# Optimization experiments

Hardware: AMD Instinct MI355X
Metric: run time of the kernel (lower is better)

## Reference

```python
import jax, jax.numpy as jnp
import numpy as np

B, P = 4, 65536
TD, HID, OUT = 32, 128, 4
RES = 256
NFREQ = 6
CD = 3 * 2 * NFREQ  # frequency encoding out dim


def setup_inputs() -> dict:
    key = jax.random.key(0)
    ks = jax.random.split(key, 12)

    def w(k, shape):
        fan_in = shape[-1]
        return jax.random.normal(k, shape, jnp.float32) / np.sqrt(fan_in)

    return {
        "triplane": jax.random.normal(ks[0], (3 * B, TD, RES, RES), jnp.float32),
        "coords": jax.random.uniform(ks[1], (B, P, 3), jnp.float32),  # inside aabb [-1,1]^3
        "w_in": w(ks[2], (HID, TD + CD)),
        "b_in": jnp.zeros((HID,), jnp.float32),
        "w_skip": w(ks[3], (HID, TD + CD)),
        "b_skip": jnp.zeros((HID,), jnp.float32),
        "w_before": w(ks[4], (2, HID, HID)),
        "b_before": jnp.zeros((2, HID), jnp.float32),
        "w_after": w(ks[5], (2, HID, HID)),
        "b_after": jnp.zeros((2, HID), jnp.float32),
        "w_out": w(ks[6], (OUT, HID)),
        "b_out": jnp.zeros((OUT,), jnp.float32),
    }


@jax.custom_vjp
def trunc_exp(x):
    return jnp.exp(x)


def _trunc_exp_fwd(x):
    return jnp.exp(x), x


def _trunc_exp_bwd(x, g):
    return (g * jnp.exp(jnp.clip(x, -15.0, 15.0)),)


trunc_exp.defvjp(_trunc_exp_fwd, _trunc_exp_bwd)


def grid_sample_bilinear(feat, gx, gy):
    # feat: [N, C, H, W]; gx, gy: [N, Q] in [-1, 1]; align_corners=True, zero padding.
    N, C, H, W = feat.shape
    ix = (gx + 1.0) * 0.5 * (W - 1)
    iy = (gy + 1.0) * 0.5 * (H - 1)
    x0 = jnp.floor(ix)
    y0 = jnp.floor(iy)
    wx1 = ix - x0
    wy1 = iy - y0
    feat_flat = feat.reshape(N, C, H * W)

    def gather(xf, yf):
        xi = xf.astype(jnp.int32)
        yi = yf.astype(jnp.int32)
        valid = ((xi >= 0) & (xi < W) & (yi >= 0) & (yi < H)).astype(feat.dtype)
        xi = jnp.clip(xi, 0, W - 1)
        yi = jnp.clip(yi, 0, H - 1)
        idx = yi * W + xi  # [N, Q]
        g = jnp.take_along_axis(feat_flat, idx[:, None, :], axis=2)  # [N, C, Q]
        return g * valid[:, None, :]

    out = (
        gather(x0, y0) * ((1 - wx1) * (1 - wy1))[:, None, :]
        + gather(x0 + 1, y0) * (wx1 * (1 - wy1))[:, None, :]
        + gather(x0, y0 + 1) * ((1 - wx1) * wy1)[:, None, :]
        + gather(x0 + 1, y0 + 1) * (wx1 * wy1)[:, None, :]
    )
    return out  # [N, C, Q]


def freq_encode(x):
    # x: [B, P, 3] in [0, 1]; NeRF-style frequency encoding (tcnn 'Frequency').
    freqs = (2.0 ** jnp.arange(NFREQ, dtype=x.dtype)) * jnp.pi  # [NFREQ]
    ang = x[..., :, None] * freqs  # [B, P, 3, NFREQ]
    enc = jnp.concatenate([jnp.sin(ang), jnp.cos(ang)], axis=-1)  # [B, P, 3, 2*NFREQ]
    return enc.reshape(x.shape[0], x.shape[1], CD)


def reference(triplane, coords, w_in, b_in, w_skip, b_skip, w_before, b_before,
              w_after, b_after, w_out, b_out):
    aabb_min = jnp.full((3,), -1.0, jnp.float32)
    aabb_max = jnp.full((3,), 1.0, jnp.float32)

    scaled = 2.0 * (coords - aabb_min) / (aabb_max - aabb_min) - 1.0  # [-1,1]
    norm = (coords - aabb_min) / (aabb_max - aabb_min)  # [0,1]
    selector = jnp.all((norm > 0.0) & (norm < 1.0), axis=-1)  # [B, P]

    # planes: xy=(x,y), xz=(x,z), zy=(y,z); stacked per batch -> [3B, P, 2]
    coords_xy = scaled[:, :, (0, 1)]
    coords_xz = scaled[:, :, (0, 2)]
    coords_zy = scaled[:, :, (1, 2)]
    grid = jnp.stack([coords_xy, coords_xz, coords_zy], axis=1).reshape(3 * B, P, 2)

    feats = grid_sample_bilinear(triplane, grid[..., 0], grid[..., 1])  # [3B, TD, P]
    feats = feats.transpose(0, 2, 1).reshape(B, 3, P, TD).sum(axis=1)  # [B, P, TD]

    h = jnp.concatenate([freq_encode(norm), feats], axis=-1)  # [B, P, CD+TD]

    lin = lambda x, w, b: jnp.einsum("bpf,hf->bph", x, w) + b
    x = jax.nn.relu(lin(h, w_in, b_in))
    for i in range(w_before.shape[0]):
        x = jax.nn.relu(lin(x, w_before[i], b_before[i]))
    x = x + jax.nn.relu(lin(h, w_skip, b_skip))
    for i in range(w_after.shape[0]):
        x = jax.nn.relu(lin(x, w_after[i], b_after[i]))
    x = lin(x, w_out, b_out)  # [B, P, 4]

    rgb = jax.nn.sigmoid(x[..., :3])
    density = trunc_exp(x[..., 3:4] - 1.0) * selector[..., None].astype(x.dtype)
    return rgb, density
```

## Files before the change

kernel.cpp:

```cpp
#include <hip/hip_runtime.h>
#include <stdint.h>

typedef short short8 __attribute__((ext_vector_type(8)));
typedef float floatx16 __attribute__((ext_vector_type(16)));
typedef unsigned int uint32;

#define NPTS (4 * 65536)
#define RGB_OFF (NPTS * 3)

__device__ __forceinline__ uint16_t bf_rne(float f) {
  uint32 u = __float_as_uint(f);
  u += 0x7FFFu + ((u >> 16) & 1u);
  return (uint16_t)(u >> 16);
}
__device__ __forceinline__ uint32 pack2(float a, float b) {
  return __builtin_amdgcn_perm(__float_as_uint(b) + 0x8000u,
                               __float_as_uint(a) + 0x8000u, 0x07060302u);
}
__device__ __forceinline__ float bf_lo(uint32 u) { return __uint_as_float(u << 16); }
__device__ __forceinline__ float bf_hi(uint32 u) { return __uint_as_float(u & 0xFFFF0000u); }
__device__ __forceinline__ void swap32(uint32& a, uint32& b) {
  asm("v_permlane32_swap_b32 %0, %1" : "+v"(a), "+v"(b));
}
__device__ __forceinline__ void gacc(const uint16_t* p, float w, float* acc) {
  uint4 q = *(const uint4*)p;
  acc[0] += w * bf_lo(q.x);
  acc[1] += w * bf_hi(q.x);
  acc[2] += w * bf_lo(q.y);
  acc[3] += w * bf_hi(q.y);
  acc[4] += w * bf_lo(q.z);
  acc[5] += w * bf_hi(q.z);
  acc[6] += w * bf_lo(q.w);
  acc[7] += w * bf_hi(q.w);
}

__global__ __launch_bounds__(256) void k_prep(
    const float* __restrict__ tri, uint16_t* __restrict__ out, int ntr,
    const float* __restrict__ w_in, const float* __restrict__ w_skip,
    const float* __restrict__ w_before, const float* __restrict__ w_after,
    const float* __restrict__ w_out, const float* __restrict__ b_in,
    const float* __restrict__ b_skip, const float* __restrict__ b_before,
    const float* __restrict__ b_after, const float* __restrict__ b_out,
    uint16_t* __restrict__ wpack, float* __restrict__ bpack) {
  const int bx = blockIdx.x;
  if (bx < ntr) {
    const size_t P = (size_t)bx * 256 + threadIdx.x;
    const int n = (int)(P >> 16);
    const int rem = (int)(P & 65535);
    const float* src = tri + ((size_t)n << 21) + rem;
    uint32 q[16];
#pragma unroll
    for (int c = 0; c < 16; ++c) {
      float a = src[(size_t)(2 * c) << 16];
      float b = src[(size_t)(2 * c + 1) << 16];
      q[c] = pack2(a, b);
    }
    uint4* dst = (uint4*)(out + P * 32);
    dst[0] = make_uint4(q[0], q[1], q[2], q[3]);
    dst[1] = make_uint4(q[4], q[5], q[6], q[7]);
    dst[2] = make_uint4(q[8], q[9], q[10], q[11]);
    dst[3] = make_uint4(q[12], q[13], q[14], q[15]);
    return;
  }
  const int blk = bx - ntr;
  if (blk >= 44) {
    for (int t = threadIdx.x; t < 800; t += 256) {
      int l, idx;
      if (t < 768) { l = t >> 7; idx = t & 127; }
      else { l = 6; idx = t - 768; }
      int mt = idx >> 5, rem = idx & 31;
      int half = rem >> 4, r = rem & 15;
      int f = mt * 32 + (r & 3) + 8 * (r >> 2) + 4 * half;
      float v;
      switch (l) {
        case 0: v = b_in[f]; break;
        case 1: v = b_before[f]; break;
        case 2: v = b_before[128 + f]; break;
        case 3: v = b_skip[f]; break;
        case 4: v = b_after[f]; break;
        case 5: v = b_after[128 + f]; break;
        default: v = (f < 4) ? b_out[f] : 0.0f; break;
      }
      bpack[l * 128 + idx] = v;
    }
    return;
  }
  const int w = blk * 4 + (threadIdx.x >> 6);
  const int L = threadIdx.x & 63;
  int lay, mt, k;
  if (w < 20)      { lay = 0; mt = w / 5;        k = w - mt * 5; }
  else if (w < 52) { int u = w - 20;  lay = 1; mt = u >> 3; k = u & 7; }
  else if (w < 84) { int u = w - 52;  lay = 2; mt = u >> 3; k = u & 7; }
  else if (w < 104){ int u = w - 84;  lay = 3; mt = u / 5;  k = u - mt * 5; }
  else if (w < 136){ int u = w - 104; lay = 4; mt = u >> 3; k = u & 7; }
  else if (w < 168){ int u = w - 136; lay = 5; mt = u >> 3; k = u & 7; }
  else             { lay = 6; mt = 0; k = w - 168; }
  const float* W;
  int insk = 0;
  switch (lay) {
    case 0: W = w_in; insk = 1; break;
    case 1: W = w_before; break;
    case 2: W = w_before + 16384; break;
    case 3: W = w_skip; insk = 1; break;
    case 4: W = w_after; break;
    case 5: W = w_after + 16384; break;
    default: W = w_out; break;
  }
  const int frow = mt * 32 + (L & 31);
  const int kbase = k * 16 + (L >> 5) * 8;
  uint16_t h[8];
#pragma unroll
  for (int j = 0; j < 8; ++j) {
    int kl = kbase + j;
    float v;
    if (insk) {
      int col = (kl < 32) ? (36 + kl) : ((kl < 68) ? (kl - 32) : -1);
      v = (col < 0) ? 0.0f : W[frow * 68 + col];
    } else if (lay == 6) {
      v = (frow < 4) ? W[frow * 128 + kl] : 0.0f;
    } else {
      v = W[frow * 128 + kl];
    }
    h[j] = bf_rne(v);
  }
  uint4 q;
  q.x = (uint32)h[0] | ((uint32)h[1] << 16);
  q.y = (uint32)h[2] | ((uint32)h[3] << 16);
  q.z = (uint32)h[4] | ((uint32)h[5] << 16);
  q.w = (uint32)h[6] | ((uint32)h[7] << 16);
  *(uint4*)(wpack + (size_t)w * 512 + L * 8) = q;
}

__device__ __forceinline__ void gather_encode(const uint16_t* __restrict__ trit,
                                              const float* __restrict__ coords,
                                              int pg, int kh, uint4* hq,
                                              bool* selp) {
  float cx = coords[pg * 3 + 0], cy = coords[pg * 3 + 1], cz = coords[pg * 3 + 2];
  float f1x = cx + 1.0f, f1y = cy + 1.0f, f1z = cz + 1.0f;
  float nx = f1x * 0.5f, ny = f1y * 0.5f, nz = f1z * 0.5f;
  float sx = f1x - 1.0f, sy = f1y - 1.0f, sz = f1z - 1.0f;
  *selp = (nx > 0.f) & (nx < 1.f) & (ny > 0.f) & (ny < 1.f) & (nz > 0.f) & (nz < 1.f);
  const int b = pg >> 16;
  float acc[16];
#pragma unroll
  for (int j = 0; j < 16; ++j) acc[j] = 0.f;
#pragma unroll
  for (int pl = 0; pl < 3; ++pl) {
    float gx = (pl == 2) ? sy : sx;
    float gy = (pl == 0) ? sy : sz;
    float ix = ((gx + 1.0f) * 0.5f) * 255.0f;
    float iy = ((gy + 1.0f) * 0.5f) * 255.0f;
    float x0f = floorf(ix), y0f = floorf(iy);
    float wx = ix - x0f, wy = iy - y0f;
    float vx0 = (x0f >= 0.0f && x0f < 256.0f) ? 1.f : 0.f;
    float vx1 = (x0f >= -1.0f && x0f < 255.0f) ? 1.f : 0.f;
    float vy0 = (y0f >= 0.0f && y0f < 256.0f) ? 1.f : 0.f;
    float vy1 = (y0f >= -1.0f && y0f < 255.0f) ? 1.f : 0.f;
    int x0 = min(max((int)x0f, 0), 255), x1 = min(max((int)x0f + 1, 0), 255);
    int y0 = min(max((int)y0f, 0), 255), y1 = min(max((int)y0f + 1, 0), 255);
    float w00 = (1.f - wx) * (1.f - wy) * vx0 * vy0;
    float w10 = wx * (1.f - wy) * vx1 * vy0;
    float w01 = (1.f - wx) * wy * vx0 * vy1;
    float w11 = wx * wy * vx1 * vy1;
    const int n = 3 * b + pl;
    const uint16_t* cb = trit + ((size_t)n << 21) + kh * 8;
    size_t o00 = (size_t)(y0 * 256 + x0) << 5, o10 = (size_t)(y0 * 256 + x1) << 5;
    size_t o01 = (size_t)(y1 * 256 + x0) << 5, o11 = (size_t)(y1 * 256 + x1) << 5;
    gacc(cb + o00, w00, acc); gacc(cb + 16 + o00, w00, acc + 8);
    gacc(cb + o10, w10, acc); gacc(cb + 16 + o10, w10, acc + 8);
    gacc(cb + o01, w01, acc); gacc(cb + 16 + o01, w01, acc + 8);
    gacc(cb + o11, w11, acc); gacc(cb + 16 + o11, w11, acc + 8);
  }
  hq[0] = make_uint4(pack2(acc[0], acc[1]), pack2(acc[2], acc[3]),
                     pack2(acc[4], acc[5]), pack2(acc[6], acc[7]));
  hq[1] = make_uint4(pack2(acc[8], acc[9]), pack2(acc[10], acc[11]),
                     pack2(acc[12], acc[13]), pack2(acc[14], acc[15]));
  float sv[3][6], cv[3][6];
#pragma unroll
  for (int d = 0; d < 3; ++d) {
    float nd = (d == 0) ? nx : (d == 1) ? ny : nz;
#pragma unroll
    for (int k = 0; k < 6; ++k) {
      float rev = nd * (0.5f * (float)(1 << k));
      float r = rev - rintf(rev);
      sv[d][k] = __builtin_amdgcn_sinf(r);
      cv[d][k] = __builtin_amdgcn_cosf(r);
    }
  }
  if (kh == 0) {
    hq[2] = make_uint4(pack2(sv[0][0], sv[0][1]), pack2(sv[0][2], sv[0][3]),
                       pack2(sv[0][4], sv[0][5]), pack2(cv[0][0], cv[0][1]));
    hq[3] = make_uint4(pack2(sv[1][4], sv[1][5]), pack2(cv[1][0], cv[1][1]),
                       pack2(cv[1][2], cv[1][3]), pack2(cv[1][4], cv[1][5]));
    hq[4] = make_uint4(pack2(cv[2][2], cv[2][3]), pack2(cv[2][4], cv[2][5]), 0u, 0u);
  } else {
    hq[2] = make_uint4(pack2(cv[0][2], cv[0][3]), pack2(cv[0][4], cv[0][5]),
                       pack2(sv[1][0], sv[1][1]), pack2(sv[1][2], sv[1][3]));
    hq[3] = make_uint4(pack2(sv[2][0], sv[2][1]), pack2(sv[2][2], sv[2][3]),
                       pack2(sv[2][4], sv[2][5]), pack2(cv[2][0], cv[2][1]));
    hq[4] = make_uint4(0u, 0u, 0u, 0u);
  }
}

template <int BASE, int LAY, int Ks>
__device__ __forceinline__ void mfma_block(floatx16* a, const short8* bin,
                                           const uint16_t* __restrict__ wpack,
                                           const float* __restrict__ bpack, int L,
                                           int kh) {
#pragma unroll
  for (int mt = 0; mt < 4; ++mt) {
    const float4* bp = (const float4*)(bpack + LAY * 128 + mt * 32 + kh * 16);
#pragma unroll
    for (int g = 0; g < 4; ++g) {
      float4 v = bp[g];
      a[mt][4 * g + 0] = v.x; a[mt][4 * g + 1] = v.y;
      a[mt][4 * g + 2] = v.z; a[mt][4 * g + 3] = v.w;
    }
  }
  const uint16_t* wp = wpack + (size_t)BASE * 512 + L * 8;
#pragma unroll
  for (int k = 0; k < Ks; ++k) {
    short8 w0 = *(const short8*)(wp + (size_t)(0 * Ks + k) * 512);
    short8 w1 = *(const short8*)(wp + (size_t)(1 * Ks + k) * 512);
    short8 w2 = *(const short8*)(wp + (size_t)(2 * Ks + k) * 512);
    short8 w3 = *(const short8*)(wp + (size_t)(3 * Ks + k) * 512);
    a[0] = __builtin_amdgcn_mfma_f32_32x32x16_bf16(w0, bin[k], a[0], 0, 0, 0);
    a[1] = __builtin_amdgcn_mfma_f32_32x32x16_bf16(w1, bin[k], a[1], 0, 0, 0);
    a[2] = __builtin_amdgcn_mfma_f32_32x32x16_bf16(w2, bin[k], a[2], 0, 0, 0);
    a[3] = __builtin_amdgcn_mfma_f32_32x32x16_bf16(w3, bin[k], a[3], 0, 0, 0);
  }
}

template <int BASE, int LAY, int Ks>
__device__ __forceinline__ void layer_dense(const short8* bin, short8* bout,
                                            const uint16_t* __restrict__ wpack,
                                            const float* __restrict__ bpack, int L,
                                            int kh) {
  floatx16 a[4];
  mfma_block<BASE, LAY, Ks>(a, bin, wpack, bpack, L, kh);
#pragma unroll
  for (int f = 0; f < 8; ++f) {
    const int mt = f >> 1, s = f & 1;
    uint32 q0a = pack2(fmaxf(a[mt][8 * s + 0], 0.f), fmaxf(a[mt][8 * s + 1], 0.f));
    uint32 q0b = pack2(fmaxf(a[mt][8 * s + 2], 0.f), fmaxf(a[mt][8 * s + 3], 0.f));
    uint32 q1a = pack2(fmaxf(a[mt][8 * s + 4], 0.f), fmaxf(a[mt][8 * s + 5], 0.f));
    uint32 q1b = pack2(fmaxf(a[mt][8 * s + 6], 0.f), fmaxf(a[mt][8 * s + 7], 0.f));
    swap32(q0a, q1a);
    swap32(q0b, q1b);
    bout[f] = __builtin_bit_cast(short8, make_uint4(q0a, q0b, q1a, q1b));
  }
}

template <int BASE, int LAY, int Ks>
__device__ __forceinline__ void layer_skip(const short8* hin, short8* bio,
                                           const uint16_t* __restrict__ wpack,
                                           const float* __restrict__ bpack, int L,
                                           int kh) {
  floatx16 a[4];
  mfma_block<BASE, LAY, Ks>(a, hin, wpack, bpack, L, kh);
#pragma unroll
  for (int f = 0; f < 8; ++f) {
    const int mt = f >> 1, s = f & 1;
    uint4 old = __builtin_bit_cast(uint4, bio[f]);
    uint32 uA = old.x, uB = old.y, uC = old.z, uD = old.w;
    swap32(uA, uC);
    swap32(uB, uD);
    float r0 = fmaxf(a[mt][8 * s + 0], 0.f) + bf_lo(uA);
    float r1 = fmaxf(a[mt][8 * s + 1], 0.f) + bf_hi(uA);
    float r2 = fmaxf(a[mt][8 * s + 2], 0.f) + bf_lo(uB);
    float r3 = fmaxf(a[mt][8 * s + 3], 0.f) + bf_hi(uB);
    float r4 = fmaxf(a[mt][8 * s + 4], 0.f) + bf_lo(uC);
    float r5 = fmaxf(a[mt][8 * s + 5], 0.f) + bf_hi(uC);
    float r6 = fmaxf(a[mt][8 * s + 6], 0.f) + bf_lo(uD);
    float r7 = fmaxf(a[mt][8 * s + 7], 0.f) + bf_hi(uD);
    uint32 q0a = pack2(r0, r1), q0b = pack2(r2, r3);
    uint32 q1a = pack2(r4, r5), q1b = pack2(r6, r7);
    swap32(q0a, q1a);
    swap32(q0b, q1b);
    bio[f] = __builtin_bit_cast(short8, make_uint4(q0a, q0b, q1a, q1b));
  }
}

__device__ __forceinline__ void mlp_body(const short8* hf, bool sel,
                                         const uint16_t* __restrict__ wpack,
                                         const float* __restrict__ bpack,
                                         float* __restrict__ dout, int L, int kh,
                                         int pg) {
  short8 bf[8];
  layer_dense<0, 0, 5>(hf, bf, wpack, bpack, L, kh);
  layer_dense<20, 1, 8>(bf, bf, wpack, bpack, L, kh);
  layer_dense<52, 2, 8>(bf, bf, wpack, bpack, L, kh);
  layer_skip<84, 3, 5>(hf, bf, wpack, bpack, L, kh);
  layer_dense<104, 4, 8>(bf, bf, wpack, bpack, L, kh);
  layer_dense<136, 5, 8>(bf, bf, wpack, bpack, L, kh);

  floatx16 a;
  const float4* bp = (const float4*)(bpack + 768 + kh * 16);
#pragma unroll
  for (int g = 0; g < 4; ++g) {
    float4 v = bp[g];
    a[4 * g + 0] = v.x; a[4 * g + 1] = v.y; a[4 * g + 2] = v.z; a[4 * g + 3] = v.w;
  }
  const uint16_t* wp = wpack + (size_t)168 * 512 + L * 8;
#pragma unroll
  for (int k = 0; k < 8; ++k) {
    short8 af = *(const short8*)(wp + (size_t)k * 512);
    a = __builtin_amdgcn_mfma_f32_32x32x16_bf16(af, bf[k], a, 0, 0, 0);
  }
  if (kh == 0) {
    const float l2e = 1.44269504f;
    float r0 = 1.0f / (1.0f + exp2f(-l2e * a[0]));
    float r1 = 1.0f / (1.0f + exp2f(-l2e * a[1]));
    float r2 = 1.0f / (1.0f + exp2f(-l2e * a[2]));
    float dens = exp2f((a[3] - 1.0f) * l2e) * (sel ? 1.0f : 0.0f);
    dout[pg * 3 + 0] = r0;
    dout[pg * 3 + 1] = r1;
    dout[pg * 3 + 2] = r2;
    dout[RGB_OFF + pg] = dens;
  }
}

__global__ __launch_bounds__(256, 3) void k_main(
    const uint16_t* __restrict__ trit, const float* __restrict__ trif,
    const float* __restrict__ coords, const uint16_t* __restrict__ wpack,
    const float* __restrict__ bpack, float* __restrict__ dout, int fast) {
  const int t = threadIdx.x;
  const int L = t & 63;
  const int kh = L >> 5;
  const int p = (t >> 6) * 32 + (L & 31);
  const int pg = blockIdx.x * 128 + p;

  short8 hf[5];
  bool sel;
  if (fast) {
    uint4 hq[5];
    gather_encode(trit, coords, pg, kh, hq, &sel);
#pragma unroll
    for (int f = 0; f < 5; ++f) hf[f] = __builtin_bit_cast(short8, hq[f]);
  } else {
    float cx = coords[pg * 3 + 0], cy = coords[pg * 3 + 1], cz = coords[pg * 3 + 2];
    float f1x = cx + 1.0f, f1y = cy + 1.0f, f1z = cz + 1.0f;
    float nx = f1x * 0.5f, ny = f1y * 0.5f, nz = f1z * 0.5f;
    float sx = f1x - 1.0f, sy = f1y - 1.0f, sz = f1z - 1.0f;
    sel = (nx > 0.f) & (nx < 1.f) & (ny > 0.f) & (ny < 1.f) & (nz > 0.f) & (nz < 1.f);
    const int b = pg >> 16;
    float acc[16];
#pragma unroll
    for (int j = 0; j < 16; ++j) acc[j] = 0.f;
#pragma unroll
    for (int pl = 0; pl < 3; ++pl) {
      float gx = (pl == 2) ? sy : sx;
      float gy = (pl == 0) ? sy : sz;
      float ix = ((gx + 1.0f) * 0.5f) * 255.0f;
      float iy = ((gy + 1.0f) * 0.5f) * 255.0f;
      float x0f = floorf(ix), y0f = floorf(iy);
      float wx = ix - x0f, wy = iy - y0f;
      float vx0 = (x0f >= 0.0f && x0f < 256.0f) ? 1.f : 0.f;
      float vx1 = (x0f >= -1.0f && x0f < 255.0f) ? 1.f : 0.f;
      float vy0 = (y0f >= 0.0f && y0f < 256.0f) ? 1.f : 0.f;
      float vy1 = (y0f >= -1.0f && y0f < 255.0f) ? 1.f : 0.f;
      int x0 = min(max((int)x0f, 0), 255), x1 = min(max((int)x0f + 1, 0), 255);
      int y0 = min(max((int)y0f, 0), 255), y1 = min(max((int)y0f + 1, 0), 255);
      float w00 = (1.f - wx) * (1.f - wy) * vx0 * vy0;
      float w10 = wx * (1.f - wy) * vx1 * vy0;
      float w01 = (1.f - wx) * wy * vx0 * vy1;
      float w11 = wx * wy * vx1 * vy1;
      const int n = 3 * b + pl;
      const float* basef = trif + (((size_t)n * 32) << 16);
#pragma unroll
      for (int j = 0; j < 8; ++j) {
        const float* c0p = basef + (((size_t)(kh * 8 + j)) << 16);
        const float* c1p = basef + (((size_t)(16 + kh * 8 + j)) << 16);
        acc[j] += w00 * c0p[y0 * 256 + x0] + w10 * c0p[y0 * 256 + x1] +
                  w01 * c0p[y1 * 256 + x0] + w11 * c0p[y1 * 256 + x1];
        acc[8 + j] += w00 * c1p[y0 * 256 + x0] + w10 * c1p[y0 * 256 + x1] +
                      w01 * c1p[y1 * 256 + x0] + w11 * c1p[y1 * 256 + x1];
      }
    }
    hf[0] = __builtin_bit_cast(
        short8, make_uint4(pack2(acc[0], acc[1]), pack2(acc[2], acc[3]),
                           pack2(acc[4], acc[5]), pack2(acc[6], acc[7])));
    hf[1] = __builtin_bit_cast(
        short8, make_uint4(pack2(acc[8], acc[9]), pack2(acc[10], acc[11]),
                           pack2(acc[12], acc[13]), pack2(acc[14], acc[15])));
    float sv[3][6], cv[3][6];
#pragma unroll
    for (int d = 0; d < 3; ++d) {
      float nd = (d == 0) ? nx : (d == 1) ? ny : nz;
#pragma unroll
      for (int k = 0; k < 6; ++k) {
        float rev = nd * (0.5f * (float)(1 << k));
        float r = rev - rintf(rev);
        sv[d][k] = __builtin_amdgcn_sinf(r);
        cv[d][k] = __builtin_amdgcn_cosf(r);
      }
    }
    if (kh == 0) {
      hf[2] = __builtin_bit_cast(
          short8, make_uint4(pack2(sv[0][0], sv[0][1]), pack2(sv[0][2], sv[0][3]),
                             pack2(sv[0][4], sv[0][5]), pack2(cv[0][0], cv[0][1])));
      hf[3] = __builtin_bit_cast(
          short8, make_uint4(pack2(sv[1][4], sv[1][5]), pack2(cv[1][0], cv[1][1]),
                             pack2(cv[1][2], cv[1][3]), pack2(cv[1][4], cv[1][5])));
      hf[4] = __builtin_bit_cast(
          short8, make_uint4(pack2(cv[2][2], cv[2][3]), pack2(cv[2][4], cv[2][5]), 0u, 0u));
    } else {
      hf[2] = __builtin_bit_cast(
          short8, make_uint4(pack2(cv[0][2], cv[0][3]), pack2(cv[0][4], cv[0][5]),
                             pack2(sv[1][0], sv[1][1]), pack2(sv[1][2], sv[1][3])));
      hf[3] = __builtin_bit_cast(
          short8, make_uint4(pack2(sv[2][0], sv[2][1]), pack2(sv[2][2], sv[2][3]),
                             pack2(sv[2][4], sv[2][5]), pack2(cv[2][0], cv[2][1])));
      hf[4] = __builtin_bit_cast(short8, make_uint4(0u, 0u, 0u, 0u));
    }
  }
  mlp_body(hf, sel, wpack, bpack, dout, L, kh, pg);
}

extern "C" void kernel_launch(void* const* d_in, const int* in_sizes, int n_in,
                              void* d_out, int out_size, void* d_ws, size_t ws_size,
                              hipStream_t stream) {
  const float* tri = (const float*)d_in[0];
  const float* coords = (const float*)d_in[1];
  const float* w_in = (const float*)d_in[2];
  const float* b_in = (const float*)d_in[3];
  const float* w_skip = (const float*)d_in[4];
  const float* b_skip = (const float*)d_in[5];
  const float* w_bef = (const float*)d_in[6];
  const float* b_bef = (const float*)d_in[7];
  const float* w_aft = (const float*)d_in[8];
  const float* b_aft = (const float*)d_in[9];
  const float* w_out = (const float*)d_in[10];
  const float* b_out = (const float*)d_in[11];
  const size_t TRI_B = (size_t)12 * 256 * 256 * 32 * 2;
  const size_t WP_B = (size_t)176 * 1024;
  const size_t BP_B = 3200;
  char* ws = (char*)d_ws;
  const int fast = (ws_size >= TRI_B + WP_B + BP_B) ? 1 : 0;
  uint16_t* trit;
  uint16_t* wpk;
  float* bpk;
  if (fast) {
    trit = (uint16_t*)ws;
    wpk = (uint16_t*)(ws + TRI_B);
    bpk = (float*)(ws + TRI_B + WP_B);
  } else {
    trit = (uint16_t*)ws;
    wpk = (uint16_t*)ws;
    bpk = (float*)(ws + WP_B);
  }
  const int ntr = fast ? 3072 : 0;
  k_prep<<<dim3(ntr + 45), dim3(256), 0, stream>>>(
      tri, trit, ntr, w_in, w_skip, w_bef, w_aft, w_out, b_in, b_skip, b_bef,
      b_aft, b_out, wpk, bpk);
  k_main<<<dim3(2048), dim3(256), 0, stream>>>(trit, tri, coords, wpk, bpk,
                                               (float*)d_out, fast);
}
```

Measured before the change: 274.4 us.

## Stage MLP weight fragments through shared memory in phases per block

Packed bf16 MLP weights are copied cooperatively into a 52 KB LDS buffer in several phases, and MFMA operand fragments are read from LDS instead of from global memory. Each of the 4 waves previously fetched the same weight fragments from global/L2 separately. The change adds several __syncthreads barriers and about 52 KB of LDS per block, which may limit occupancy below the 3 blocks per CU requested by the launch bounds. The first stage is issued before the gather so that the copy can overlap with it.

```diff
diff --git a/kernel.cpp b/kernel.cpp
--- a/kernel.cpp
+++ b/kernel.cpp
@@ -129,6 +129,147 @@
   q.z = (uint32)h[4] | ((uint32)h[5] << 16);
   q.w = (uint32)h[6] | ((uint32)h[7] << 16);
   *(uint4*)(wpack + (size_t)w * 512 + L * 8) = q;
+}
+
+template <int NFRAG>
+__device__ __forceinline__ void stage(const uint16_t* __restrict__ wp_base,
+                                      uint16_t* __restrict__ wbuf, int t) {
+#pragma unroll
+  for (int i = 0; i < NFRAG * 64 / 256; ++i) {
+    const int g = t + i * 256;
+    uint4 v = *(const uint4*)(wp_base + g * 8);
+    *(uint4*)(wbuf + g * 8) = v;
+  }
+}
+
+template <int LAY, int Ks>
+__device__ __forceinline__ void mfma_block(floatx16* a, const short8* bin,
+                                           const uint16_t* __restrict__ wbuf,
+                                           const float* __restrict__ bpack, int L,
+                                           int kh) {
+#pragma unroll
+  for (int mt = 0; mt < 4; ++mt) {
+    const float4* bp = (const float4*)(bpack + LAY * 128 + mt * 32 + kh * 16);
+#pragma unroll
+    for (int g = 0; g < 4; ++g) {
+      float4 v = bp[g];
+      a[mt][4 * g + 0] = v.x; a[mt][4 * g + 1] = v.y;
+      a[mt][4 * g + 2] = v.z; a[mt][4 * g + 3] = v.w;
+    }
+  }
+  const uint16_t* wp = wbuf + L * 8;
+#pragma unroll
+  for (int k = 0; k < Ks; ++k) {
+    short8 w0 = *(const short8*)(wp + (size_t)(0 * Ks + k) * 512);
+    short8 w1 = *(const short8*)(wp + (size_t)(1 * Ks + k) * 512);
+    short8 w2 = *(const short8*)(wp + (size_t)(2 * Ks + k) * 512);
+    short8 w3 = *(const short8*)(wp + (size_t)(3 * Ks + k) * 512);
+    a[0] = __builtin_amdgcn_mfma_f32_32x32x16_bf16(w0, bin[k], a[0], 0, 0, 0);
+    a[1] = __builtin_amdgcn_mfma_f32_32x32x16_bf16(w1, bin[k], a[1], 0, 0, 0);
+    a[2] = __builtin_amdgcn_mfma_f32_32x32x16_bf16(w2, bin[k], a[2], 0, 0, 0);
+    a[3] = __builtin_amdgcn_mfma_f32_32x32x16_bf16(w3, bin[k], a[3], 0, 0, 0);
+  }
+}
+
+template <int LAY, int Ks>
+__device__ __forceinline__ void layer_dense(const short8* bin, short8* bout,
+                                            const uint16_t* __restrict__ wbuf,
+                                            const float* __restrict__ bpack, int L,
+                                            int kh) {
+  floatx16 a[4];
+  mfma_block<LAY, Ks>(a, bin, wbuf, bpack, L, kh);
+#pragma unroll
+  for (int f = 0; f < 8; ++f) {
+    const int mt = f >> 1, s = f & 1;
+    uint32 q0a = pack2(fmaxf(a[mt][8 * s + 0], 0.f), fmaxf(a[mt][8 * s + 1], 0.f));
+    uint32 q0b = pack2(fmaxf(a[mt][8 * s + 2], 0.f), fmaxf(a[mt][8 * s + 3], 0.f));
+    uint32 q1a = pack2(fmaxf(a[mt][8 * s + 4], 0.f), fmaxf(a[mt][8 * s + 5], 0.f));
+    uint32 q1b = pack2(fmaxf(a[mt][8 * s + 6], 0.f), fmaxf(a[mt][8 * s + 7], 0.f));
+    swap32(q0a, q1a);
+    swap32(q0b, q1b);
+    bout[f] = __builtin_bit_cast(short8, make_uint4(q0a, q0b, q1a, q1b));
+  }
+}
+
+template <int LAY, int Ks>
+__device__ __forceinline__ void layer_skip(const short8* hin, short8* bio,
+                                           const uint16_t* __restrict__ wbuf,
+                                           const float* __restrict__ bpack, int L,
+                                           int kh) {
+  floatx16 a[4];
+  mfma_block<LAY, Ks>(a, hin, wbuf, bpack, L, kh);
+#pragma unroll
+  for (int f = 0; f < 8; ++f) {
+    const int mt = f >> 1, s = f & 1;
+    uint4 old = __builtin_bit_cast(uint4, bio[f]);
+    uint32 uA = old.x, uB = old.y, uC = old.z, uD = old.w;
+    swap32(uA, uC);
+    swap32(uB, uD);
+    float r0 = fmaxf(a[mt][8 * s + 0], 0.f) + bf_lo(uA);
+    float r1 = fmaxf(a[mt][8 * s + 1], 0.f) + bf_hi(uA);
+    float r2 = fmaxf(a[mt][8 * s + 2], 0.f) + bf_lo(uB);
+    float r3 = fmaxf(a[mt][8 * s + 3], 0.f) + bf_hi(uB);
+    float r4 = fmaxf(a[mt][8 * s + 4], 0.f) + bf_lo(uC);
+    float r5 = fmaxf(a[mt][8 * s + 5], 0.f) + bf_hi(uC);
+    float r6 = fmaxf(a[mt][8 * s + 6], 0.f) + bf_lo(uD);
+    float r7 = fmaxf(a[mt][8 * s + 7], 0.f) + bf_hi(uD);
+    uint32 q0a = pack2(r0, r1), q0b = pack2(r2, r3);
+    uint32 q1a = pack2(r4, r5), q1b = pack2(r6, r7);
+    swap32(q0a, q1a);
+    swap32(q0b, q1b);
+    bio[f] = __builtin_bit_cast(short8, make_uint4(q0a, q0b, q1a, q1b));
+  }
+}
+
+__device__ __forceinline__ void mlp_body(const short8* hf, bool sel,
+                                         const uint16_t* __restrict__ wpack,
+                                         const float* __restrict__ bpack,
+                                         uint16_t* __restrict__ wbuf,
+                                         float* __restrict__ dout, int t, int L,
+                                         int kh, int pg) {
+  short8 bf[8];
+  __syncthreads();
+  layer_dense<0, 5>(hf, bf, wbuf, bpack, L, kh);
+  layer_dense<1, 8>(bf, bf, wbuf + (size_t)20 * 512, bpack, L, kh);
+  __syncthreads();
+  stage<52>(wpack + (size_t)52 * 512, wbuf, t);
+  __syncthreads();
+  layer_dense<2, 8>(bf, bf, wbuf, bpack, L, kh);
+  layer_skip<3, 5>(hf, bf, wbuf + (size_t)32 * 512, bpack, L, kh);
+  __syncthreads();
+  stage<32>(wpack + (size_t)104 * 512, wbuf, t);
+  stage<8>(wpack + (size_t)168 * 512, wbuf + (size_t)32 * 512, t);
+  __syncthreads();
+  layer_dense<4, 8>(bf, bf, wbuf, bpack, L, kh);
+  __syncthreads();
+  stage<32>(wpack + (size_t)136 * 512, wbuf, t);
+  __syncthreads();
+  layer_dense<5, 8>(bf, bf, wbuf, bpack, L, kh);
+
+  floatx16 a;
+  const float4* bp = (const float4*)(bpack + 768 + kh * 16);
+#pragma unroll
+  for (int g = 0; g < 4; ++g) {
+    float4 v = bp[g];
+    a[4 * g + 0] = v.x; a[4 * g + 1] = v.y; a[4 * g + 2] = v.z; a[4 * g + 3] = v.w;
+  }
+  const uint16_t* wp = wbuf + (size_t)32 * 512 + L * 8;
+#pragma unroll
+  for (int k = 0; k < 8; ++k) {
+    short8 af = *(const short8*)(wp + (size_t)k * 512);
+    a = __builtin_amdgcn_mfma_f32_32x32x16_bf16(af, bf[k], a, 0, 0, 0);
+  }
+  if (kh == 0) {
+    const float l2e = 1.44269504f;
+    float r0 = 1.0f / (1.0f + exp2f(-l2e * a[0]));
+    float r1 = 1.0f / (1.0f + exp2f(-l2e * a[1]));
+    float r2 = 1.0f / (1.0f + exp2f(-l2e * a[2]));
+    float dens = exp2f((a[3] - 1.0f) * l2e) * (sel ? 1.0f : 0.0f);
+    dout[pg * 3 + 0] = r0;
+    dout[pg * 3 + 1] = r1;
+    dout[pg * 3 + 2] = r2;
+    dout[RGB_OFF + pg] = dens;
+  }
 }
 
 __device__ __forceinline__ void gather_encode(const uint16_t* __restrict__ trit,
@@ -202,133 +343,18 @@
   }
 }
 
-template <int BASE, int LAY, int Ks>
-__device__ __forceinline__ void mfma_block(floatx16* a, const short8* bin,
-                                           const uint16_t* __restrict__ wpack,
-                                           const float* __restrict__ bpack, int L,
-                                           int kh) {
-#pragma unroll
-  for (int mt = 0; mt < 4; ++mt) {
-    const float4* bp = (const float4*)(bpack + LAY * 128 + mt * 32 + kh * 16);
-#pragma unroll
-    for (int g = 0; g < 4; ++g) {
-      float4 v = bp[g];
-      a[mt][4 * g + 0] = v.x; a[mt][4 * g + 1] = v.y;
-      a[mt][4 * g + 2] = v.z; a[mt][4 * g + 3] = v.w;
-    }
-  }
-  const uint16_t* wp = wpack + (size_t)BASE * 512 + L * 8;
-#pragma unroll
-  for (int k = 0; k < Ks; ++k) {
-    short8 w0 = *(const short8*)(wp + (size_t)(0 * Ks + k) * 512);
-    short8 w1 = *(const short8*)(wp + (size_t)(1 * Ks + k) * 512);
-    short8 w2 = *(const short8*)(wp + (size_t)(2 * Ks + k) * 512);
-    short8 w3 = *(const short8*)(wp + (size_t)(3 * Ks + k) * 512);
-    a[0] = __builtin_amdgcn_mfma_f32_32x32x16_bf16(w0, bin[k], a[0], 0, 0, 0);
-    a[1] = __builtin_amdgcn_mfma_f32_32x32x16_bf16(w1, bin[k], a[1], 0, 0, 0);
-    a[2] = __builtin_amdgcn_mfma_f32_32x32x16_bf16(w2, bin[k], a[2], 0, 0, 0);
-    a[3] = __builtin_amdgcn_mfma_f32_32x32x16_bf16(w3, bin[k], a[3], 0, 0, 0);
-  }
-}
-
-template <int BASE, int LAY, int Ks>
-__device__ __forceinline__ void layer_dense(const short8* bin, short8* bout,
-                                            const uint16_t* __restrict__ wpack,
-                                            const float* __restrict__ bpack, int L,
-                                            int kh) {
-  floatx16 a[4];
-  mfma_block<BASE, LAY, Ks>(a, bin, wpack, bpack, L, kh);
-#pragma unroll
-  for (int f = 0; f < 8; ++f) {
-    const int mt = f >> 1, s = f & 1;
-    uint32 q0a = pack2(fmaxf(a[mt][8 * s + 0], 0.f), fmaxf(a[mt][8 * s + 1], 0.f));
-    uint32 q0b = pack2(fmaxf(a[mt][8 * s + 2], 0.f), fmaxf(a[mt][8 * s + 3], 0.f));
-    uint32 q1a = pack2(fmaxf(a[mt][8 * s + 4], 0.f), fmaxf(a[mt][8 * s + 5], 0.f));
-    uint32 q1b = pack2(fmaxf(a[mt][8 * s + 6], 0.f), fmaxf(a[mt][8 * s + 7], 0.f));
-    swap32(q0a, q1a);
-    swap32(q0b, q1b);
-    bout[f] = __builtin_bit_cast(short8, make_uint4(q0a, q0b, q1a, q1b));
-  }
-}
-
-template <int BASE, int LAY, int Ks>
-__device__ __forceinline__ void layer_skip(const short8* hin, short8* bio,
-                                           const uint16_t* __restrict__ wpack,
-                                           const float* __restrict__ bpack, int L,
-                                           int kh) {
-  floatx16 a[4];
-  mfma_block<BASE, LAY, Ks>(a, hin, wpack, bpack, L, kh);
-#pragma unroll
-  for (int f = 0; f < 8; ++f) {
-    const int mt = f >> 1, s = f & 1;
-    uint4 old = __builtin_bit_cast(uint4, bio[f]);
-    uint32 uA = old.x, uB = old.y, uC = old.z, uD = old.w;
-    swap32(uA, uC);
-    swap32(uB, uD);
-    float r0 = fmaxf(a[mt][8 * s + 0], 0.f) + bf_lo(uA);
-    float r1 = fmaxf(a[mt][8 * s + 1], 0.f) + bf_hi(uA);
-    float r2 = fmaxf(a[mt][8 * s + 2], 0.f) + bf_lo(uB);
-    float r3 = fmaxf(a[mt][8 * s + 3], 0.f) + bf_hi(uB);
-    float r4 = fmaxf(a[mt][8 * s + 4], 0.f) + bf_lo(uC);
-    float r5 = fmaxf(a[mt][8 * s + 5], 0.f) + bf_hi(uC);
-    float r6 = fmaxf(a[mt][8 * s + 6], 0.f) + bf_lo(uD);
-    float r7 = fmaxf(a[mt][8 * s + 7], 0.f) + bf_hi(uD);
-    uint32 q0a = pack2(r0, r1), q0b = pack2(r2, r3);
-    uint32 q1a = pack2(r4, r5), q1b = pack2(r6, r7);
-    swap32(q0a, q1a);
-    swap32(q0b, q1b);
-    bio[f] = __builtin_bit_cast(short8, make_uint4(q0a, q0b, q1a, q1b));
-  }
-}
-
-__device__ __forceinline__ void mlp_body(const short8* hf, bool sel,
-                                         const uint16_t* __restrict__ wpack,
-                                         const float* __restrict__ bpack,
-                                         float* __restrict__ dout, int L, int kh,
-                                         int pg) {
-  short8 bf[8];
-  layer_dense<0, 0, 5>(hf, bf, wpack, bpack, L, kh);
-  layer_dense<20, 1, 8>(bf, bf, wpack, bpack, L, kh);
-  layer_dense<52, 2, 8>(bf, bf, wpack, bpack, L, kh);
-  layer_skip<84, 3, 5>(hf, bf, wpack, bpack, L, kh);
-  layer_dense<104, 4, 8>(bf, bf, wpack, bpack, L, kh);
-  layer_dense<136, 5, 8>(bf, bf, wpack, bpack, L, kh);
-
-  floatx16 a;
-  const float4* bp = (const float4*)(bpack + 768 + kh * 16);
-#pragma unroll
-  for (int g = 0; g < 4; ++g) {
-    float4 v = bp[g];
-    a[4 * g + 0] = v.x; a[4 * g + 1] = v.y; a[4 * g + 2] = v.z; a[4 * g + 3] = v.w;
-  }
-  const uint16_t* wp = wpack + (size_t)168 * 512 + L * 8;
-#pragma unroll
-  for (int k = 0; k < 8; ++k) {
-    short8 af = *(const short8*)(wp + (size_t)k * 512);
-    a = __builtin_amdgcn_mfma_f32_32x32x16_bf16(af, bf[k], a, 0, 0, 0);
-  }
-  if (kh == 0) {
-    const float l2e = 1.44269504f;
-    float r0 = 1.0f / (1.0f + exp2f(-l2e * a[0]));
-    float r1 = 1.0f / (1.0f + exp2f(-l2e * a[1]));
-    float r2 = 1.0f / (1.0f + exp2f(-l2e * a[2]));
-    float dens = exp2f((a[3] - 1.0f) * l2e) * (sel ? 1.0f : 0.0f);
-    dout[pg * 3 + 0] = r0;
-    dout[pg * 3 + 1] = r1;
-    dout[pg * 3 + 2] = r2;
-    dout[RGB_OFF + pg] = dens;
-  }
-}
-
 __global__ __launch_bounds__(256, 3) void k_main(
     const uint16_t* __restrict__ trit, const float* __restrict__ trif,
     const float* __restrict__ coords, const uint16_t* __restrict__ wpack,
     const float* __restrict__ bpack, float* __restrict__ dout, int fast) {
+  __shared__ __align__(16) uint16_t wbuf[26624];
   const int t = threadIdx.x;
   const int L = t & 63;
   const int kh = L >> 5;
   const int p = (t >> 6) * 32 + (L & 31);
   const int pg = blockIdx.x * 128 + p;
+
+  stage<52>(wpack, wbuf, t);
 
   short8 hf[5];
   bool sel;
@@ -414,7 +440,7 @@
       hf[4] = __builtin_bit_cast(short8, make_uint4(0u, 0u, 0u, 0u));
     }
   }
-  mlp_body(hf, sel, wpack, bpack, dout, L, kh, pg);
+  mlp_body(hf, sel, wpack, bpack, wbuf, dout, t, L, kh, pg);
 }
 
 extern "C" void kernel_launch(void* const* d_in, const int* in_sizes, int n_in,
```

Result: no change. 269.3 us (-1.9%).
